# Optimization experiments

Hardware: AMD Instinct MI355X
Metric: run time of the kernel (lower is better)

The kernel has to match this reference:

```python
import jax, jax.numpy as jnp
import numpy as np

N_HEADS = 16
WINDOW = 256


def setup_inputs() -> dict:
    key = jax.random.key(0)
    ks = jax.random.split(key, 6)
    B, S, D = 2, 2048, 1024
    std = 0.02
    x = jax.random.normal(ks[0], (B, S, D), dtype=jnp.float32)
    wq = jax.random.normal(ks[1], (D, D), dtype=jnp.float32) * std
    wk = jax.random.normal(ks[2], (D, D), dtype=jnp.float32) * std
    wv = jax.random.normal(ks[3], (D, D), dtype=jnp.float32) * std
    wo = jax.random.normal(ks[4], (D, D), dtype=jnp.float32) * std
    bq = jnp.zeros((D,), jnp.float32)
    bk = jnp.zeros((D,), jnp.float32)
    bv = jnp.zeros((D,), jnp.float32)
    bo = jnp.zeros((D,), jnp.float32)
    return {"x": x, "wq": wq, "bq": bq, "wk": wk, "bk": bk,
            "wv": wv, "bv": bv, "wo": wo, "bo": bo}


def _sliding_window_bias(seq_len: int) -> jnp.ndarray:
    # allowed iff |i - j| <= WINDOW  ->  0.0, else -inf  (matches torch loop mask)
    i = jnp.arange(seq_len)[:, None]
    j = jnp.arange(seq_len)[None, :]
    allowed = jnp.abs(i - j) <= WINDOW
    return jnp.where(allowed, 0.0, -jnp.inf).astype(jnp.float32)


def reference(x, wq, bq, wk, bk, wv, bv, wo, bo):
    B, S, D = x.shape
    H = N_HEADS
    dh = D // H
    scale = dh ** -0.5
    # nn.Linear: y = x @ W^T + b
    q = (x @ wq.T + bq).reshape(B, S, H, dh).transpose(0, 2, 1, 3)  # [B,H,S,dh]
    k = (x @ wk.T + bk).reshape(B, S, H, dh).transpose(0, 2, 1, 3)
    v = (x @ wv.T + bv).reshape(B, S, H, dh).transpose(0, 2, 1, 3)
    scores = jnp.einsum('bhqd,bhkd->bhqk', q, k) * scale  # [B,H,S,S]
    scores = scores + _sliding_window_bias(S)[None, None]
    attn = jax.nn.softmax(scores, axis=-1)
    out = jnp.einsum('bhqk,bhkd->bhqd', attn, v)  # [B,H,S,dh]
    out = out.transpose(0, 2, 1, 3).reshape(B, S, D)
    return out @ wo.T + bo
```

## Files before the change

### kernel.cpp

```cpp
#include <hip/hip_runtime.h>
#include <stdint.h>

static constexpr int Ss = 2048;
static constexpr int Dd = 1024;
static constexpr int Hh = 16;
static constexpr int DH = 64;

typedef short bf16x8 __attribute__((ext_vector_type(8)));
typedef float f32x4 __attribute__((ext_vector_type(4)));

#define LOG2E 1.4426950408889634f

__device__ __forceinline__ uint16_t f2bf(float f) {
  uint32_t u = __builtin_bit_cast(uint32_t, f);
  u += 0x7fffu + ((u >> 16) & 1u);
  return (uint16_t)(u >> 16);
}
__device__ __forceinline__ float bf2f(uint16_t h) {
  uint32_t u = ((uint32_t)h) << 16;
  return __builtin_bit_cast(float, u);
}

template <int CTRL>
__device__ __forceinline__ float dppf(float x) {
  return __builtin_bit_cast(float,
      __builtin_amdgcn_update_dpp(0, __builtin_bit_cast(int, x), CTRL, 0xF, 0xF, true));
}
__device__ __forceinline__ float rowmax16(float v) {
  v = fmaxf(v, dppf<0x128>(v));
  v = fmaxf(v, dppf<0x124>(v));
  v = fmaxf(v, dppf<0x122>(v));
  v = fmaxf(v, dppf<0x121>(v));
  return v;
}
__device__ __forceinline__ float rowsum16(float v) {
  v += dppf<0x128>(v);
  v += dppf<0x124>(v);
  v += dppf<0x122>(v);
  v += dppf<0x121>(v);
  return v;
}
__device__ __forceinline__ float fexp2(float x) { return __builtin_amdgcn_exp2f(x); }

#define GAS(p) ((const __attribute__((address_space(1))) uint32_t*)(p))
#define LAS(p) ((__attribute__((address_space(3))) uint32_t*)(p))

__global__ void cvt_f32_bf16(const float* __restrict__ in, uint16_t* __restrict__ out, int n4) {
  int i = blockIdx.x * blockDim.x + threadIdx.x;
  if (i < n4) {
    float4 v = reinterpret_cast<const float4*>(in)[i];
    ushort4 o;
    o.x = f2bf(v.x); o.y = f2bf(v.y); o.z = f2bf(v.z); o.w = f2bf(v.w);
    reinterpret_cast<ushort4*>(out)[i] = o;
  }
}

__global__ void cvt_w4(const float* __restrict__ w0, const float* __restrict__ w1,
                       const float* __restrict__ w2, const float* __restrict__ w3,
                       uint16_t* __restrict__ o0, uint16_t* __restrict__ o1,
                       uint16_t* __restrict__ o2, uint16_t* __restrict__ o3, int n4) {
  int y = blockIdx.y;
  const float* in = (y == 0) ? w0 : (y == 1) ? w1 : (y == 2) ? w2 : w3;
  uint16_t* out = (y == 0) ? o0 : (y == 1) ? o1 : (y == 2) ? o2 : o3;
  int i = blockIdx.x * blockDim.x + threadIdx.x;
  if (i < n4) {
    float4 v = reinterpret_cast<const float4*>(in)[i];
    ushort4 o;
    o.x = f2bf(v.x); o.y = f2bf(v.y); o.z = f2bf(v.z); o.w = f2bf(v.w);
    reinterpret_cast<ushort4*>(out)[i] = o;
  }
}

template <int MODE>
__global__ __launch_bounds__(256, 2) void gemm_nt(
    const uint16_t* __restrict__ A,
    const uint16_t* __restrict__ W0, const uint16_t* __restrict__ W1, const uint16_t* __restrict__ W2,
    const float* __restrict__ b0, const float* __restrict__ b1, const float* __restrict__ b2,
    void* __restrict__ O0, void* __restrict__ O1, void* __restrict__ O2,
    int M, int N, int K) {
  __shared__ __align__(16) uint8_t ldsA[128 * 128];
  __shared__ __align__(16) uint8_t ldsB[128 * 128];

  const int tid = threadIdx.x, w = tid >> 6, lane = tid & 63;
  const int q = lane & 15, g = lane >> 4;
  const int wm = w >> 1, wn = w & 1;
  const int bx = blockIdx.x, by = blockIdx.y, z = blockIdx.z;
  const uint16_t* Wp = (z == 0) ? W0 : (z == 1) ? W1 : W2;
  const float* bp = (z == 0) ? b0 : (z == 1) ? b1 : b2;
  void* Op = (z == 0) ? O0 : (z == 1) ? O1 : O2;

  f32x4 acc[4][4] = {};

  const int nkt = K >> 6;
  for (int kt = 0; kt < nkt; ++kt) {
    const int k0 = kt << 6;
    __syncthreads();
#pragma unroll
    for (int i = 0; i < 4; ++i) {
      int Lb = w * 4096 + i * 1024 + lane * 16;
      int row = Lb >> 7, cb = Lb & 127;
      int col = (cb ^ ((row & 7) << 4)) >> 1;
      const uint16_t* srcA = A + (size_t)(bx * 128 + row) * K + k0 + col;
      __builtin_amdgcn_global_load_lds(GAS(srcA), LAS(ldsA + w * 4096 + i * 1024), 16, 0, 0);
      const uint16_t* srcB = Wp + (size_t)(by * 128 + row) * K + k0 + col;
      __builtin_amdgcn_global_load_lds(GAS(srcB), LAS(ldsB + w * 4096 + i * 1024), 16, 0, 0);
    }
    __syncthreads();

    bf16x8 af[4][2], bfg[4][2];
#pragma unroll
    for (int mi = 0; mi < 4; ++mi)
#pragma unroll
      for (int s = 0; s < 2; ++s) {
        int row = wm * 64 + mi * 16 + q;
        int cb = (16 * g + 64 * s) ^ ((row & 7) << 4);
        af[mi][s] = *(const bf16x8*)(ldsA + row * 128 + cb);
      }
#pragma unroll
    for (int ni = 0; ni < 4; ++ni)
#pragma unroll
      for (int s = 0; s < 2; ++s) {
        int row = wn * 64 + ni * 16 + q;
        int cb = (16 * g + 64 * s) ^ ((row & 7) << 4);
        bfg[ni][s] = *(const bf16x8*)(ldsB + row * 128 + cb);
      }
#pragma unroll
    for (int mi = 0; mi < 4; ++mi)
#pragma unroll
      for (int ni = 0; ni < 4; ++ni) {
        acc[mi][ni] = __builtin_amdgcn_mfma_f32_16x16x32_bf16(af[mi][0], bfg[ni][0], acc[mi][ni], 0, 0, 0);
        acc[mi][ni] = __builtin_amdgcn_mfma_f32_16x16x32_bf16(af[mi][1], bfg[ni][1], acc[mi][ni], 0, 0, 0);
      }
  }

  float bias[4];
#pragma unroll
  for (int ni = 0; ni < 4; ++ni) bias[ni] = bp[by * 128 + wn * 64 + ni * 16 + q];
#pragma unroll
  for (int mi = 0; mi < 4; ++mi)
#pragma unroll
    for (int ni = 0; ni < 4; ++ni)
#pragma unroll
      for (int r = 0; r < 4; ++r) {
        int m = bx * 128 + wm * 64 + mi * 16 + 4 * g + r;
        int n = by * 128 + wn * 64 + ni * 16 + q;
        float v = acc[mi][ni][r] + bias[ni];
        if (MODE == 0) {
          int b = m >> 11, s = m & 2047, h = n >> 6, d = n & 63;
          ((uint16_t*)Op)[(((size_t)(b * Hh + h) * Ss + s) << 6) + d] = f2bf(v);
        } else {
          ((float*)Op)[(size_t)m * N + n] = v;
        }
      }
}

__global__ __launch_bounds__(256, 2) void attn_swa(
    const uint16_t* __restrict__ Qg, const uint16_t* __restrict__ Kg,
    const uint16_t* __restrict__ Vg, uint16_t* __restrict__ Og) {
  __shared__ __align__(16) uint8_t ldsK[64 * 128];
  __shared__ __align__(16) uint8_t ldsVt[64 * 128];
  __shared__ __align__(16) uint8_t ldsP[4][2048];

  const int tid = threadIdx.x, w = tid >> 6, lane = tid & 63;
  const int q = lane & 15, g = lane >> 4;
  const int qb = blockIdx.x, bh = blockIdx.y;
  const size_t hbase = (size_t)bh * Ss * DH;
  const uint16_t* Qp = Qg + hbase;
  const uint16_t* Kp = Kg + hbase;
  const uint16_t* Vp = Vg + hbase;
  const int q0 = qb * 64;
  const int qw = q0 + w * 16;

  bf16x8 aq[2];
#pragma unroll
  for (int s = 0; s < 2; ++s) {
    bf16x8 t = *(const bf16x8*)(Qp + (size_t)(qw + q) * DH + s * 32 + g * 8);
#pragma unroll
    for (int j = 0; j < 8; ++j) {
      float f = bf2f((uint16_t)t[j]) * 0.125f;
      t[j] = (short)f2bf(f);
    }
    aq[s] = t;
  }

  f32x4 accO[4] = {};
  float mrun[4] = {-1e30f, -1e30f, -1e30f, -1e30f};
  float lrun[4] = {0.f, 0.f, 0.f, 0.f};

  const int t0 = (q0 >= 256) ? (q0 - 256) : 0;
  const int t1 = (q0 + 320 <= Ss) ? (q0 + 320) : Ss;

  for (int kb0 = t0; kb0 < t1; kb0 += 64) {
    const uint16_t* vrow = Vp + (size_t)(kb0 + lane) * DH + w * 16;
    bf16x8 v0 = *(const bf16x8*)(vrow);
    bf16x8 v1 = *(const bf16x8*)(vrow + 8);

    __syncthreads();
#pragma unroll
    for (int i = 0; i < 2; ++i) {
      int Lb = w * 2048 + i * 1024 + lane * 16;
      int row = Lb >> 7, cb = Lb & 127;
      const uint16_t* srcK = Kp + (size_t)(kb0 + row) * DH + ((cb ^ ((row & 7) << 4)) >> 1);
      __builtin_amdgcn_global_load_lds(GAS(srcK), LAS(ldsK + w * 2048 + i * 1024), 16, 0, 0);
    }
#pragma unroll
    for (int j = 0; j < 8; ++j) {
      int c0 = w * 16 + j;
      *(uint16_t*)(ldsVt + c0 * 128 + ((2 * lane) ^ ((c0 & 7) << 4))) = (uint16_t)v0[j];
      int c1 = w * 16 + 8 + j;
      *(uint16_t*)(ldsVt + c1 * 128 + ((2 * lane) ^ ((c1 & 7) << 4))) = (uint16_t)v1[j];
    }
    __syncthreads();

    f32x4 sacc[4] = {};
#pragma unroll
    for (int kb = 0; kb < 4; ++kb) {
      int row = kb * 16 + q;
#pragma unroll
      for (int s = 0; s < 2; ++s) {
        int cb = (16 * g + 64 * s) ^ ((row & 7) << 4);
        bf16x8 bk = *(const bf16x8*)(ldsK + row * 128 + cb);
        sacc[kb] = __builtin_amdgcn_mfma_f32_16x16x32_bf16(aq[s], bk, sacc[kb], 0, 0, 0);
      }
    }
    if (kb0 - q0 < -192 || kb0 - q0 > 192) {
#pragma unroll
      for (int kb = 0; kb < 4; ++kb) {
        int key = kb0 + kb * 16 + q;
#pragma unroll
        for (int r = 0; r < 4; ++r) {
          int qi = qw + 4 * g + r;
          int dd = qi - key;
          bool ok = (dd <= 256) && (dd >= -256);
          sacc[kb][r] = ok ? sacc[kb][r] : -1e30f;
        }
      }
    }
#pragma unroll
    for (int r = 0; r < 4; ++r) {
      float tm = fmaxf(fmaxf(sacc[0][r], sacc[1][r]), fmaxf(sacc[2][r], sacc[3][r]));
      tm = rowmax16(tm);
      float mnew = fmaxf(mrun[r], tm);
      float mL = mnew * LOG2E;
      float alpha = fexp2(__builtin_fmaf(mrun[r], LOG2E, -mL));
      mrun[r] = mnew;
      float p0 = fexp2(__builtin_fmaf(sacc[0][r], LOG2E, -mL));
      float p1 = fexp2(__builtin_fmaf(sacc[1][r], LOG2E, -mL));
      float p2 = fexp2(__builtin_fmaf(sacc[2][r], LOG2E, -mL));
      float p3 = fexp2(__builtin_fmaf(sacc[3][r], LOG2E, -mL));
      sacc[0][r] = p0; sacc[1][r] = p1; sacc[2][r] = p2; sacc[3][r] = p3;
      float rs = rowsum16((p0 + p1) + (p2 + p3));
      lrun[r] = lrun[r] * alpha + rs;
#pragma unroll
      for (int db = 0; db < 4; ++db) accO[db][r] *= alpha;
    }
    uint8_t* Pl = ldsP[w];
#pragma unroll
    for (int kb = 0; kb < 4; ++kb) {
      int col2 = (kb * 16 + q) * 2;
#pragma unroll
      for (int r = 0; r < 4; ++r) {
        int prow = 4 * g + r;
        *(uint16_t*)(Pl + prow * 128 + (col2 ^ ((prow & 7) << 4))) = f2bf(sacc[kb][r]);
      }
    }
    bf16x8 ap[2];
#pragma unroll
    for (int s = 0; s < 2; ++s) {
      int cb = (16 * g + 64 * s) ^ ((q & 7) << 4);
      ap[s] = *(const bf16x8*)(Pl + q * 128 + cb);
    }
#pragma unroll
    for (int db = 0; db < 4; ++db) {
      int vr = db * 16 + q;
#pragma unroll
      for (int s = 0; s < 2; ++s) {
        int cb = (64 * s + 16 * g) ^ ((vr & 7) << 4);
        bf16x8 bvf = *(const bf16x8*)(ldsVt + vr * 128 + cb);
        accO[db] = __builtin_amdgcn_mfma_f32_16x16x32_bf16(ap[s], bvf, accO[db], 0, 0, 0);
      }
    }
  }

  const int b2 = bh >> 4, h = bh & 15;
#pragma unroll
  for (int r = 0; r < 4; ++r) {
    float inv = 1.0f / lrun[r];
    int qi = qw + 4 * g + r;
    size_t rowbase = ((size_t)(b2 * Ss + qi)) * Dd + h * DH;
#pragma unroll
    for (int db = 0; db < 4; ++db) {
      Og[rowbase + db * 16 + q] = f2bf(accO[db][r] * inv);
    }
  }
}

extern "C" void kernel_launch(void* const* d_in, const int* in_sizes, int n_in,
                              void* d_out, int out_size, void* d_ws, size_t ws_size,
                              hipStream_t stream) {
  const float* x  = (const float*)d_in[0];
  const float* wq = (const float*)d_in[1];
  const float* bq = (const float*)d_in[2];
  const float* wk = (const float*)d_in[3];
  const float* bk = (const float*)d_in[4];
  const float* wv = (const float*)d_in[5];
  const float* bv = (const float*)d_in[6];
  const float* wo = (const float*)d_in[7];
  const float* bo = (const float*)d_in[8];
  float* out = (float*)d_out;

  uint8_t* ws = (uint8_t*)d_ws;
  uint16_t* xb  = (uint16_t*)(ws + (size_t)(0u  << 20));
  uint16_t* wqb = (uint16_t*)(ws + (size_t)(8u  << 20));
  uint16_t* wkb = (uint16_t*)(ws + (size_t)(10u << 20));
  uint16_t* wvb = (uint16_t*)(ws + (size_t)(12u << 20));
  uint16_t* wob = (uint16_t*)(ws + (size_t)(14u << 20));
  uint16_t* Qb  = (uint16_t*)(ws + (size_t)(16u << 20));
  uint16_t* Kb  = (uint16_t*)(ws + (size_t)(24u << 20));
  uint16_t* Vb  = (uint16_t*)(ws + (size_t)(32u << 20));
  uint16_t* AOb = (uint16_t*)(ws + (size_t)(40u << 20));

  cvt_f32_bf16<<<4096, 256, 0, stream>>>(x, xb, 1048576);
  cvt_w4<<<dim3(1024, 4), 256, 0, stream>>>(wq, wk, wv, wo, wqb, wkb, wvb, wob, 262144);

  gemm_nt<0><<<dim3(32, 8, 3), 256, 0, stream>>>(
      xb, wqb, wkb, wvb, bq, bk, bv, (void*)Qb, (void*)Kb, (void*)Vb, 4096, 1024, 1024);

  attn_swa<<<dim3(32, 32), 256, 0, stream>>>(Qb, Kb, Vb, AOb);

  gemm_nt<1><<<dim3(32, 8, 1), 256, 0, stream>>>(
      AOb, wob, wob, wob, bo, bo, bo, (void*)out, (void*)out, (void*)out, 4096, 1024, 1024);
}
```

Measured before the change: 93.54 us.

## Double-buffer attention K/V tiles, merge conversion kernels, narrow output GEMM tile

The attention kernel now double-buffers K and V in LDS. The next tile's K (async to LDS) and V (to registers) load while the current tile is computed, which removes one barrier per iteration, and launch bounds are raised to 4 blocks per CU. The two f32-to-bf16 conversion kernels are merged into one launch to save launch overhead. The output projection GEMM uses a 64-wide N tile with twice as many blocks, giving better CU fill for the 256-block grid. The extra LDS and the higher occupancy target may cause register pressure or spills in the attention kernel.

New measurement: 87.07 us. 6.9% less time.

```diff
diff --git a/kernel.cpp b/kernel.cpp
--- a/kernel.cpp
+++ b/kernel.cpp
@@ -45,41 +45,41 @@
 #define GAS(p) ((const __attribute__((address_space(1))) uint32_t*)(p))
 #define LAS(p) ((__attribute__((address_space(3))) uint32_t*)(p))
 
-__global__ void cvt_f32_bf16(const float* __restrict__ in, uint16_t* __restrict__ out, int n4) {
-  int i = blockIdx.x * blockDim.x + threadIdx.x;
-  if (i < n4) {
-    float4 v = reinterpret_cast<const float4*>(in)[i];
-    ushort4 o;
-    o.x = f2bf(v.x); o.y = f2bf(v.y); o.z = f2bf(v.z); o.w = f2bf(v.w);
-    reinterpret_cast<ushort4*>(out)[i] = o;
-  }
-}
-
-__global__ void cvt_w4(const float* __restrict__ w0, const float* __restrict__ w1,
-                       const float* __restrict__ w2, const float* __restrict__ w3,
-                       uint16_t* __restrict__ o0, uint16_t* __restrict__ o1,
-                       uint16_t* __restrict__ o2, uint16_t* __restrict__ o3, int n4) {
-  int y = blockIdx.y;
-  const float* in = (y == 0) ? w0 : (y == 1) ? w1 : (y == 2) ? w2 : w3;
-  uint16_t* out = (y == 0) ? o0 : (y == 1) ? o1 : (y == 2) ? o2 : o3;
-  int i = blockIdx.x * blockDim.x + threadIdx.x;
-  if (i < n4) {
-    float4 v = reinterpret_cast<const float4*>(in)[i];
-    ushort4 o;
-    o.x = f2bf(v.x); o.y = f2bf(v.y); o.z = f2bf(v.z); o.w = f2bf(v.w);
-    reinterpret_cast<ushort4*>(out)[i] = o;
-  }
-}
-
-template <int MODE>
+__global__ void cvt_all(const float* __restrict__ x,
+                        const float* __restrict__ w0, const float* __restrict__ w1,
+                        const float* __restrict__ w2, const float* __restrict__ w3,
+                        uint16_t* __restrict__ xb,
+                        uint16_t* __restrict__ o0, uint16_t* __restrict__ o1,
+                        uint16_t* __restrict__ o2, uint16_t* __restrict__ o3) {
+  int bid = blockIdx.x;
+  const float* in;
+  uint16_t* out;
+  int i;
+  if (bid < 4096) {
+    in = x; out = xb; i = bid * 256 + threadIdx.x;
+  } else {
+    int b2 = bid - 4096;
+    int t = b2 >> 10;
+    in = (t == 0) ? w0 : (t == 1) ? w1 : (t == 2) ? w2 : w3;
+    out = (t == 0) ? o0 : (t == 1) ? o1 : (t == 2) ? o2 : o3;
+    i = (b2 & 1023) * 256 + threadIdx.x;
+  }
+  float4 v = reinterpret_cast<const float4*>(in)[i];
+  ushort4 o;
+  o.x = f2bf(v.x); o.y = f2bf(v.y); o.z = f2bf(v.z); o.w = f2bf(v.w);
+  reinterpret_cast<ushort4*>(out)[i] = o;
+}
+
+template <int MODE, int BN>
 __global__ __launch_bounds__(256, 2) void gemm_nt(
     const uint16_t* __restrict__ A,
     const uint16_t* __restrict__ W0, const uint16_t* __restrict__ W1, const uint16_t* __restrict__ W2,
     const float* __restrict__ b0, const float* __restrict__ b1, const float* __restrict__ b2,
     void* __restrict__ O0, void* __restrict__ O1, void* __restrict__ O2,
     int M, int N, int K) {
+  constexpr int NI = BN / 32;
   __shared__ __align__(16) uint8_t ldsA[128 * 128];
-  __shared__ __align__(16) uint8_t ldsB[128 * 128];
+  __shared__ __align__(16) uint8_t ldsB[BN * 128];
 
   const int tid = threadIdx.x, w = tid >> 6, lane = tid & 63;
   const int q = lane & 15, g = lane >> 4;
@@ -89,7 +89,7 @@
   const float* bp = (z == 0) ? b0 : (z == 1) ? b1 : b2;
   void* Op = (z == 0) ? O0 : (z == 1) ? O1 : O2;
 
-  f32x4 acc[4][4] = {};
+  f32x4 acc[4][NI] = {};
 
   const int nkt = K >> 6;
   for (int kt = 0; kt < nkt; ++kt) {
@@ -102,12 +102,18 @@
       int col = (cb ^ ((row & 7) << 4)) >> 1;
       const uint16_t* srcA = A + (size_t)(bx * 128 + row) * K + k0 + col;
       __builtin_amdgcn_global_load_lds(GAS(srcA), LAS(ldsA + w * 4096 + i * 1024), 16, 0, 0);
-      const uint16_t* srcB = Wp + (size_t)(by * 128 + row) * K + k0 + col;
-      __builtin_amdgcn_global_load_lds(GAS(srcB), LAS(ldsB + w * 4096 + i * 1024), 16, 0, 0);
+    }
+#pragma unroll
+    for (int i = 0; i < BN / 32; ++i) {
+      int Lb = w * (BN * 32) + i * 1024 + lane * 16;
+      int row = Lb >> 7, cb = Lb & 127;
+      int col = (cb ^ ((row & 7) << 4)) >> 1;
+      const uint16_t* srcB = Wp + (size_t)(by * BN + row) * K + k0 + col;
+      __builtin_amdgcn_global_load_lds(GAS(srcB), LAS(ldsB + w * (BN * 32) + i * 1024), 16, 0, 0);
     }
     __syncthreads();
 
-    bf16x8 af[4][2], bfg[4][2];
+    bf16x8 af[4][2], bfg[NI][2];
 #pragma unroll
     for (int mi = 0; mi < 4; ++mi)
 #pragma unroll
@@ -117,33 +123,33 @@
         af[mi][s] = *(const bf16x8*)(ldsA + row * 128 + cb);
       }
 #pragma unroll
-    for (int ni = 0; ni < 4; ++ni)
+    for (int ni = 0; ni < NI; ++ni)
 #pragma unroll
       for (int s = 0; s < 2; ++s) {
-        int row = wn * 64 + ni * 16 + q;
+        int row = wn * (BN / 2) + ni * 16 + q;
         int cb = (16 * g + 64 * s) ^ ((row & 7) << 4);
         bfg[ni][s] = *(const bf16x8*)(ldsB + row * 128 + cb);
       }
 #pragma unroll
     for (int mi = 0; mi < 4; ++mi)
 #pragma unroll
-      for (int ni = 0; ni < 4; ++ni) {
+      for (int ni = 0; ni < NI; ++ni) {
         acc[mi][ni] = __builtin_amdgcn_mfma_f32_16x16x32_bf16(af[mi][0], bfg[ni][0], acc[mi][ni], 0, 0, 0);
         acc[mi][ni] = __builtin_amdgcn_mfma_f32_16x16x32_bf16(af[mi][1], bfg[ni][1], acc[mi][ni], 0, 0, 0);
       }
   }
 
-  float bias[4];
-#pragma unroll
-  for (int ni = 0; ni < 4; ++ni) bias[ni] = bp[by * 128 + wn * 64 + ni * 16 + q];
+  float bias[NI];
+#pragma unroll
+  for (int ni = 0; ni < NI; ++ni) bias[ni] = bp[by * BN + wn * (BN / 2) + ni * 16 + q];
 #pragma unroll
   for (int mi = 0; mi < 4; ++mi)
 #pragma unroll
-    for (int ni = 0; ni < 4; ++ni)
+    for (int ni = 0; ni < NI; ++ni)
 #pragma unroll
       for (int r = 0; r < 4; ++r) {
         int m = bx * 128 + wm * 64 + mi * 16 + 4 * g + r;
-        int n = by * 128 + wn * 64 + ni * 16 + q;
+        int n = by * BN + wn * (BN / 2) + ni * 16 + q;
         float v = acc[mi][ni][r] + bias[ni];
         if (MODE == 0) {
           int b = m >> 11, s = m & 2047, h = n >> 6, d = n & 63;
@@ -154,11 +160,11 @@
       }
 }
 
-__global__ __launch_bounds__(256, 2) void attn_swa(
+__global__ __launch_bounds__(256, 4) void attn_swa(
     const uint16_t* __restrict__ Qg, const uint16_t* __restrict__ Kg,
     const uint16_t* __restrict__ Vg, uint16_t* __restrict__ Og) {
-  __shared__ __align__(16) uint8_t ldsK[64 * 128];
-  __shared__ __align__(16) uint8_t ldsVt[64 * 128];
+  __shared__ __align__(16) uint8_t ldsK[2][64 * 128];
+  __shared__ __align__(16) uint8_t ldsVt[2][64 * 128];
   __shared__ __align__(16) uint8_t ldsP[4][2048];
 
   const int tid = threadIdx.x, w = tid >> 6, lane = tid & 63;
@@ -189,29 +195,50 @@
 
   const int t0 = (q0 >= 256) ? (q0 - 256) : 0;
   const int t1 = (q0 + 320 <= Ss) ? (q0 + 320) : Ss;
-
-  for (int kb0 = t0; kb0 < t1; kb0 += 64) {
-    const uint16_t* vrow = Vp + (size_t)(kb0 + lane) * DH + w * 16;
-    bf16x8 v0 = *(const bf16x8*)(vrow);
-    bf16x8 v1 = *(const bf16x8*)(vrow + 8);
-
-    __syncthreads();
-#pragma unroll
-    for (int i = 0; i < 2; ++i) {
-      int Lb = w * 2048 + i * 1024 + lane * 16;
-      int row = Lb >> 7, cb = Lb & 127;
-      const uint16_t* srcK = Kp + (size_t)(kb0 + row) * DH + ((cb ^ ((row & 7) << 4)) >> 1);
-      __builtin_amdgcn_global_load_lds(GAS(srcK), LAS(ldsK + w * 2048 + i * 1024), 16, 0, 0);
-    }
+  const int nt = (t1 - t0) >> 6;
+
+#pragma unroll
+  for (int i = 0; i < 2; ++i) {
+    int Lb = w * 2048 + i * 1024 + lane * 16;
+    int row = Lb >> 7, cb = Lb & 127;
+    const uint16_t* srcK = Kp + (size_t)(t0 + row) * DH + ((cb ^ ((row & 7) << 4)) >> 1);
+    __builtin_amdgcn_global_load_lds(GAS(srcK), LAS(ldsK[0] + w * 2048 + i * 1024), 16, 0, 0);
+  }
+  const uint16_t* vrow0 = Vp + (size_t)(t0 + lane) * DH + w * 16;
+  bf16x8 v0 = *(const bf16x8*)(vrow0);
+  bf16x8 v1 = *(const bf16x8*)(vrow0 + 8);
+
+  for (int t = 0; t < nt; ++t) {
+    const int kb0 = t0 + (t << 6);
+    const int cur = t & 1, nxt = cur ^ 1;
+
+    uint8_t* Vt = ldsVt[cur];
 #pragma unroll
     for (int j = 0; j < 8; ++j) {
       int c0 = w * 16 + j;
-      *(uint16_t*)(ldsVt + c0 * 128 + ((2 * lane) ^ ((c0 & 7) << 4))) = (uint16_t)v0[j];
+      *(uint16_t*)(Vt + c0 * 128 + ((2 * lane) ^ ((c0 & 7) << 4))) = (uint16_t)v0[j];
       int c1 = w * 16 + 8 + j;
-      *(uint16_t*)(ldsVt + c1 * 128 + ((2 * lane) ^ ((c1 & 7) << 4))) = (uint16_t)v1[j];
-    }
-    __syncthreads();
-
+      *(uint16_t*)(Vt + c1 * 128 + ((2 * lane) ^ ((c1 & 7) << 4))) = (uint16_t)v1[j];
+    }
+    asm volatile("s_waitcnt lgkmcnt(0)" ::: "memory");
+    __builtin_amdgcn_sched_barrier(0);
+    __builtin_amdgcn_s_barrier();
+    __builtin_amdgcn_sched_barrier(0);
+
+    if (t + 1 < nt) {
+#pragma unroll
+      for (int i = 0; i < 2; ++i) {
+        int Lb = w * 2048 + i * 1024 + lane * 16;
+        int row = Lb >> 7, cb = Lb & 127;
+        const uint16_t* srcK = Kp + (size_t)(kb0 + 64 + row) * DH + ((cb ^ ((row & 7) << 4)) >> 1);
+        __builtin_amdgcn_global_load_lds(GAS(srcK), LAS(ldsK[nxt] + w * 2048 + i * 1024), 16, 0, 0);
+      }
+      const uint16_t* vrow = Vp + (size_t)(kb0 + 64 + lane) * DH + w * 16;
+      v0 = *(const bf16x8*)(vrow);
+      v1 = *(const bf16x8*)(vrow + 8);
+    }
+
+    const uint8_t* Kl = ldsK[cur];
     f32x4 sacc[4] = {};
 #pragma unroll
     for (int kb = 0; kb < 4; ++kb) {
@@ -219,7 +246,7 @@
 #pragma unroll
       for (int s = 0; s < 2; ++s) {
         int cb = (16 * g + 64 * s) ^ ((row & 7) << 4);
-        bf16x8 bk = *(const bf16x8*)(ldsK + row * 128 + cb);
+        bf16x8 bk = *(const bf16x8*)(Kl + row * 128 + cb);
         sacc[kb] = __builtin_amdgcn_mfma_f32_16x16x32_bf16(aq[s], bk, sacc[kb], 0, 0, 0);
       }
     }
@@ -276,7 +303,7 @@
 #pragma unroll
       for (int s = 0; s < 2; ++s) {
         int cb = (64 * s + 16 * g) ^ ((vr & 7) << 4);
-        bf16x8 bvf = *(const bf16x8*)(ldsVt + vr * 128 + cb);
+        bf16x8 bvf = *(const bf16x8*)(ldsVt[cur] + vr * 128 + cb);
         accO[db] = __builtin_amdgcn_mfma_f32_16x16x32_bf16(ap[s], bvf, accO[db], 0, 0, 0);
       }
     }
@@ -320,14 +347,13 @@
   uint16_t* Vb  = (uint16_t*)(ws + (size_t)(32u << 20));
   uint16_t* AOb = (uint16_t*)(ws + (size_t)(40u << 20));
 
-  cvt_f32_bf16<<<4096, 256, 0, stream>>>(x, xb, 1048576);
-  cvt_w4<<<dim3(1024, 4), 256, 0, stream>>>(wq, wk, wv, wo, wqb, wkb, wvb, wob, 262144);
-
-  gemm_nt<0><<<dim3(32, 8, 3), 256, 0, stream>>>(
+  cvt_all<<<8192, 256, 0, stream>>>(x, wq, wk, wv, wo, xb, wqb, wkb, wvb, wob);
+
+  gemm_nt<0, 128><<<dim3(32, 8, 3), 256, 0, stream>>>(
       xb, wqb, wkb, wvb, bq, bk, bv, (void*)Qb, (void*)Kb, (void*)Vb, 4096, 1024, 1024);
 
   attn_swa<<<dim3(32, 32), 256, 0, stream>>>(Qb, Kb, Vb, AOb);
 
-  gemm_nt<1><<<dim3(32, 8, 1), 256, 0, stream>>>(
+  gemm_nt<1, 64><<<dim3(32, 16, 1), 256, 0, stream>>>(
       AOb, wob, wob, wob, bo, bo, bo, (void*)out, (void*)out, (void*)out, 4096, 1024, 1024);
 }
```
